# Optimization experiments

Measured on AMD Instinct MI355X. Metric: run time of the kernel, lower is better.

The kernel has to match this reference:

```python
import jax, jax.numpy as jnp
import numpy as np

HEAD_DIM = 128
MROPE_SECTION = (16, 24, 24)  # sums to HEAD_DIM // 2
ROPE_THETA = 1000000.0
NEG_INF = -2.3819763e38


def _mrope_cos_sin(positions, theta, mrope_section, head_dim):
    # positions: [3, B, T] int; returns cos, sin of shape [B, T, head_dim]
    half = head_dim // 2
    inv_freq = 1.0 / (theta ** (jnp.arange(half, dtype=jnp.float32) * 2.0 / head_dim))
    angles = positions.astype(jnp.float32)[..., None] * inv_freq  # [3, B, T, half]
    sec = np.cumsum([0] + list(mrope_section))
    # pick temporal/height/width channel per frequency band
    angles_sel = jnp.concatenate(
        [angles[j, ..., sec[j]:sec[j + 1]] for j in range(3)], axis=-1
    )  # [B, T, half]
    cos = jnp.cos(angles_sel)
    sin = jnp.sin(angles_sel)
    cos = jnp.concatenate([cos, cos], axis=-1)  # [B, T, head_dim]
    sin = jnp.concatenate([sin, sin], axis=-1)
    return cos, sin


def _apply_rope(x, cos, sin):
    # x: [B, T, n, H]; cos/sin: [B, T, H]
    half = x.shape[-1] // 2
    x1, x2 = x[..., :half], x[..., half:]
    rot = jnp.concatenate([-x2, x1], axis=-1)
    return x * cos[:, :, None, :] + rot * sin[:, :, None, :]


def setup_inputs() -> dict:
    key = jax.random.key(0)
    ks = jax.random.split(key, 8)
    B, T, D = 2, 512, 3584
    N, K, H = 28, 4, 128
    S_CACHE = 3584
    S = S_CACHE + T
    x = jax.random.normal(ks[0], (B, T, D), dtype=jnp.float32)
    wq = jax.random.normal(ks[1], (N, D, H), dtype=jnp.float32) * (D ** -0.5)
    wk = jax.random.normal(ks[2], (K, D, H), dtype=jnp.float32) * (D ** -0.5)
    wv = jax.random.normal(ks[3], (K, D, H), dtype=jnp.float32) * (D ** -0.5)
    wo = jax.random.normal(ks[4], (N, H, D), dtype=jnp.float32) * ((N * H) ** -0.5)
    cache_k = jax.random.normal(ks[5], (B, S_CACHE, K, H), dtype=jnp.float32)
    cache_v = jax.random.normal(ks[6], (B, S_CACHE, K, H), dtype=jnp.float32)
    # positions continue after the cache; all 3 mrope channels identical (text)
    pos1d = S_CACHE + jnp.arange(T, dtype=jnp.int32)
    positions = jnp.broadcast_to(pos1d[None, None, :], (3, B, T))
    # mask: full visibility into cache, causal within the new block
    causal = jnp.tril(jnp.ones((T, T), dtype=bool))
    attn_mask = jnp.concatenate(
        [jnp.ones((T, S_CACHE), dtype=bool), causal], axis=-1
    )[None, None].repeat(B, axis=0)  # [B, 1, T, S]
    return {"x": x, "positions": positions, "attn_mask": attn_mask,
            "cache_k": cache_k, "cache_v": cache_v,
            "wq": wq, "wk": wk, "wv": wv, "wo": wo}


def reference(x, positions, attn_mask, cache_k, cache_v, wq, wk, wv, wo):
    N, K, H = wq.shape[0], wk.shape[0], wq.shape[2]
    G = N // K
    q = jnp.einsum('BTD,NDH->BTNH', x, wq)
    k = jnp.einsum('BSD,KDH->BSKH', x, wk)
    v = jnp.einsum('BSD,KDH->BSKH', x, wv)
    cos, sin = _mrope_cos_sin(positions, ROPE_THETA, MROPE_SECTION, H)
    q = _apply_rope(q, cos, sin)
    k = _apply_rope(k, cos, sin)
    q = q * (H ** -0.5)
    k = jnp.concatenate([cache_k, k], axis=1)  # [B, S, K, H]
    v = jnp.concatenate([cache_v, v], axis=1)
    cached_k, cached_v = k, v
    B, T = q.shape[0], q.shape[1]
    qg = q.reshape(B, T, K, G, H)
    # GQA: broadcast each kv head over its G query-head group (same math as repeat_kv)
    logits = jnp.einsum('BTKGH,BSKH->BKGTS', qg, k,
                        preferred_element_type=jnp.float32)
    masked = jnp.where(attn_mask[:, :, None, :, :], logits, NEG_INF)
    probs = jax.nn.softmax(masked, axis=-1).astype(x.dtype)
    encoded = jnp.einsum('BKGTS,BSKH->BTKGH', probs, v).reshape(B, T, N, H)
    out = jnp.einsum('BTNH,NHD->BTD', encoded, wo)
    return out, cached_k, cached_v
```

## Files before the change

kernel.cpp:

```cpp
#include <hip/hip_runtime.h>
#include <cstdint>
#include <cstddef>
#include <cmath>

typedef __bf16 bf16;
typedef __bf16 bf16x8 __attribute__((ext_vector_type(8)));
typedef float f32x4 __attribute__((ext_vector_type(4)));

__device__ __forceinline__ f32x4 mfma_bf16(bf16x8 a, bf16x8 b, f32x4 c) {
  return __builtin_amdgcn_mfma_f32_16x16x32_bf16(a, b, c, 0, 0, 0);
}

union U8 { bf16 h[8]; uint4 u; };
__device__ __forceinline__ uint4 cvt8(float4 a, float4 b) {
  U8 t;
  t.h[0] = (bf16)a.x; t.h[1] = (bf16)a.y; t.h[2] = (bf16)a.z; t.h[3] = (bf16)a.w;
  t.h[4] = (bf16)b.x; t.h[5] = (bf16)b.y; t.h[6] = (bf16)b.z; t.h[7] = (bf16)b.w;
  return t.u;
}

__device__ __forceinline__ bf16x8 ones8() {
  union { uint4 u; bf16x8 h; } t;
  t.u = make_uint4(0x3F803F80u, 0x3F803F80u, 0x3F803F80u, 0x3F803F80u);
  return t.h;
}

__device__ __forceinline__ void gload_lds16(const bf16* g, bf16* l) {
  __builtin_amdgcn_global_load_lds((const __attribute__((address_space(1))) void*)g,
                                   (__attribute__((address_space(3))) void*)l, 16, 0, 0);
}

__global__ __launch_bounds__(256) void prep(const float* __restrict__ ck,
                                            const float* __restrict__ cv,
                                            float* __restrict__ cko,
                                            float* __restrict__ cvo,
                                            bf16* __restrict__ kb_t,
                                            const float* __restrict__ x,
                                            bf16* __restrict__ xb,
                                            const int* __restrict__ pos,
                                            float* __restrict__ cosb,
                                            float* __restrict__ sinb) {
  size_t idx = (size_t)blockIdx.x * 256 + threadIdx.x;
  size_t e = idx * 8;
  size_t b = e / 1835008u, re = e % 1835008u;
  size_t de = b * 2097152u + re;
  float4 k0 = *(const float4*)(ck + e), k1 = *(const float4*)(ck + e + 4);
  float4 v0 = *(const float4*)(cv + e), v1 = *(const float4*)(cv + e + 4);
  *(float4*)(cko + de) = k0; *(float4*)(cko + de + 4) = k1;
  *(float4*)(cvo + de) = v0; *(float4*)(cvo + de + 4) = v1;
  {
    int s = (int)(re >> 9);
    int rem = (int)(re & 511);
    int khh = rem >> 7, h0 = rem & 127;
    size_t dk = ((size_t)(b * 4 + khh) * 128 + (s >> 5)) * 4096 + (size_t)(s & 31) * 128 + h0;
    *(uint4*)(kb_t + dk) = cvt8(k0, k1);
  }
  *(uint4*)(xb + e) = cvt8(*(const float4*)(x + e), *(const float4*)(x + e + 4));
  if (idx < 65536) {
    int m = (int)(idx >> 6), i = (int)(idx & 63);
    int j = (i < 16) ? 0 : ((i < 40) ? 1 : 2);
    float p = (float)pos[j * 1024 + m];
    float invf = (float)exp((double)i * -0.21586735246819178);
    float a = p * invf;
    cosb[m * 64 + i] = cosf(a);
    sinb[m * 64 + i] = sinf(a);
  }
}

__global__ __launch_bounds__(256) void transpose_f2b(const float* __restrict__ src,
                                                     bf16* __restrict__ dst,
                                                     int R, int C) {
  const size_t ms = (size_t)R * C;
  const float* s = src + (size_t)blockIdx.z * ms;
  bf16* d = dst + (size_t)blockIdx.z * ms;
  const int c0 = blockIdx.x * 64, r0 = blockIdx.y * 64;
  __shared__ bf16 tile[64 * 72];
  const int tid = threadIdx.x;
#pragma unroll
  for (int it = 0; it < 2; ++it) {
    int slot = tid + it * 256;
    int r = slot >> 3, c8 = slot & 7;
    const float* p = s + (size_t)(r0 + r) * C + c0 + c8 * 8;
    *(uint4*)(tile + r * 72 + c8 * 8) = cvt8(*(const float4*)p, *(const float4*)(p + 4));
  }
  __syncthreads();
#pragma unroll
  for (int it = 0; it < 2; ++it) {
    int slot = tid + it * 256;
    int c = slot >> 3, r8 = slot & 7;
    U8 tmp;
#pragma unroll
    for (int jj = 0; jj < 8; ++jj) tmp.h[jj] = tile[(r8 * 8 + jj) * 72 + c];
    *(uint4*)(d + (size_t)(c0 + c) * R + r0 + r8 * 8) = tmp.u;
  }
}

__global__ __launch_bounds__(256) void transpose_qkv(const float* __restrict__ wq,
                                                     const float* __restrict__ wk,
                                                     const float* __restrict__ wv,
                                                     bf16* __restrict__ dst) {
  const size_t ms = (size_t)3584 * 128;
  const int z = blockIdx.z;
  const float* s = (z < 28) ? wq + (size_t)z * ms
                 : (z < 32) ? wk + (size_t)(z - 28) * ms
                            : wv + (size_t)(z - 32) * ms;
  bf16* d = dst + (size_t)z * ms;
  const int c0 = blockIdx.x * 64, r0 = blockIdx.y * 64;
  __shared__ bf16 tile[64 * 72];
  const int tid = threadIdx.x;
#pragma unroll
  for (int it = 0; it < 2; ++it) {
    int slot = tid + it * 256;
    int r = slot >> 3, c8 = slot & 7;
    const float* p = s + (size_t)(r0 + r) * 128 + c0 + c8 * 8;
    *(uint4*)(tile + r * 72 + c8 * 8) = cvt8(*(const float4*)p, *(const float4*)(p + 4));
  }
  __syncthreads();
#pragma unroll
  for (int it = 0; it < 2; ++it) {
    int slot = tid + it * 256;
    int c = slot >> 3, r8 = slot & 7;
    U8 tmp;
#pragma unroll
    for (int jj = 0; jj < 8; ++jj) tmp.h[jj] = tile[(r8 * 8 + jj) * 72 + c];
    *(uint4*)(d + (size_t)(c0 + c) * 3584 + r0 + r8 * 8) = tmp.u;
  }
}

__global__ __launch_bounds__(256) void transpose_v(const float* __restrict__ cvo,
                                                   bf16* __restrict__ vt_t) {
  const int b = blockIdx.z >> 2, kh = blockIdx.z & 3;
  const int s0 = blockIdx.x * 64, h0 = blockIdx.y * 64;
  __shared__ bf16 tile[64 * 72];
  const int tid = threadIdx.x;
#pragma unroll
  for (int it = 0; it < 2; ++it) {
    int slot = tid + it * 256;
    int r = slot >> 3, c8 = slot & 7;
    const float* p = cvo + (size_t)((b * 4096 + s0 + r) * 4 + kh) * 128 + h0 + c8 * 8;
    *(uint4*)(tile + r * 72 + c8 * 8) = cvt8(*(const float4*)p, *(const float4*)(p + 4));
  }
  __syncthreads();
#pragma unroll
  for (int it = 0; it < 2; ++it) {
    int slot = tid + it * 256;
    int c = slot >> 3, r8 = slot & 7;
    U8 tmp;
#pragma unroll
    for (int jj = 0; jj < 8; ++jj) tmp.h[jj] = tile[(r8 * 8 + jj) * 72 + c];
    int s = s0 + r8 * 8;
    *(uint4*)(vt_t + ((size_t)((b * 4 + kh) * 128 + (s >> 5))) * 4096 +
              (size_t)(h0 + c) * 32 + (s & 31)) = tmp.u;
  }
}

template <int MODE>
__global__ __launch_bounds__(256) void gemm128(
    const bf16* __restrict__ A, const bf16* __restrict__ Bt,
    bf16* __restrict__ q_ws, float* __restrict__ cko, bf16* __restrict__ kb_t,
    float* __restrict__ cvo, const float* __restrict__ cosb,
    const float* __restrict__ sinb, float* __restrict__ outp) {
  const int cb = blockIdx.x;
  const int m0 = blockIdx.y * 128;
  const int tid = threadIdx.x;
  const int wave = tid >> 6, lane = tid & 63;
  const int c16 = lane & 15, q4 = lane >> 4;
  __shared__ bf16 lA[2][128 * 64];
  __shared__ bf16 lB[2][128 * 64];

  int offA[2][2], offB[8][2];
#pragma unroll
  for (int i = 0; i < 2; ++i) {
    int rA = wave * 32 + i * 16 + c16;
#pragma unroll
    for (int kk = 0; kk < 2; ++kk) offA[i][kk] = rA * 64 + (kk * 4 + q4) * 8;
  }
#pragma unroll
  for (int j = 0; j < 8; ++j) {
    int rB = j * 16 + c16;
#pragma unroll
    for (int kk = 0; kk < 2; ++kk) offB[j][kk] = rB * 64 + (kk * 4 + q4) * 8;
  }

  f32x4 acc[2][8];
#pragma unroll
  for (int i = 0; i < 2; ++i)
#pragma unroll
    for (int j = 0; j < 8; ++j) acc[i][j] = (f32x4){0.f, 0.f, 0.f, 0.f};

#pragma unroll
  for (int it = 0; it < 4; ++it) {
    int slot = tid + it * 256;
    gload_lds16(A + (size_t)(m0 + (slot >> 3)) * 3584 + (slot & 7) * 8, &lA[0][slot * 8]);
    gload_lds16(Bt + (size_t)(cb * 128 + (slot >> 3)) * 3584 + (slot & 7) * 8, &lB[0][slot * 8]);
  }
  __syncthreads();

  for (int k0 = 0; k0 < 3584; k0 += 64) {
    const int cur = (k0 >> 6) & 1;
    if (k0 + 64 < 3584) {
#pragma unroll
      for (int it = 0; it < 4; ++it) {
        int slot = tid + it * 256;
        gload_lds16(A + (size_t)(m0 + (slot >> 3)) * 3584 + k0 + 64 + (slot & 7) * 8,
                    &lA[cur ^ 1][slot * 8]);
        gload_lds16(Bt + (size_t)(cb * 128 + (slot >> 3)) * 3584 + k0 + 64 + (slot & 7) * 8,
                    &lB[cur ^ 1][slot * 8]);
      }
    }
#pragma unroll
    for (int kk = 0; kk < 2; ++kk) {
      bf16x8 av0 = *(const bf16x8*)(&lA[cur][offA[0][kk]]);
      bf16x8 av1 = *(const bf16x8*)(&lA[cur][offA[1][kk]]);
#pragma unroll
      for (int j = 0; j < 8; ++j) {
        bf16x8 bv = *(const bf16x8*)(&lB[cur][offB[j][kk]]);
        acc[0][j] = mfma_bf16(av0, bv, acc[0][j]);
        acc[1][j] = mfma_bf16(av1, bv, acc[1][j]);
      }
    }
    __syncthreads();
  }

  if (MODE == 1) {
#pragma unroll
    for (int i = 0; i < 2; ++i) {
      int mb = m0 + wave * 32 + i * 16 + q4 * 4;
#pragma unroll
      for (int r = 0; r < 4; ++r) {
        size_t rowoff = (size_t)(mb + r) * 3584 + cb * 128;
#pragma unroll
        for (int j = 0; j < 8; ++j) outp[rowoff + j * 16 + c16] = acc[i][j][r];
      }
    }
    return;
  }

  const int head = cb;
#pragma unroll
  for (int i = 0; i < 2; ++i) {
    int mb = m0 + wave * 32 + i * 16 + q4 * 4;
#pragma unroll
    for (int r = 0; r < 4; ++r) {
      int m = mb + r;
      int bb = m >> 9, tt = m & 511;
      if (head < 32) {
        const float* cp = cosb + m * 64;
        const float* sp = sinb + m * 64;
#pragma unroll
        for (int j = 0; j < 4; ++j) {
          int h = j * 16 + c16;
          float c = cp[h], s = sp[h];
          float v1 = acc[i][j][r], v2 = acc[i][j + 4][r];
          float o1 = v1 * c - v2 * s;
          float o2 = v2 * c + v1 * s;
          if (head < 28) {
            const float QS = 0.08838834764831845f;
            size_t base = ((size_t)m * 28 + head) * 128;
            q_ws[base + h] = (bf16)(o1 * QS);
            q_ws[base + h + 64] = (bf16)(o2 * QS);
          } else {
            int sg = 3584 + tt;
            size_t base = ((size_t)((bb * 4096 + sg) * 4 + (head - 28))) * 128;
            cko[base + h] = o1;
            cko[base + h + 64] = o2;
            size_t bt = ((size_t)(bb * 4 + (head - 28)) * 128 + (sg >> 5)) * 4096 +
                        (size_t)(sg & 31) * 128;
            kb_t[bt + h] = (bf16)o1;
            kb_t[bt + h + 64] = (bf16)o2;
          }
        }
      } else {
        size_t base = ((size_t)((bb * 4096 + 3584 + tt) * 4 + (head - 32))) * 128;
#pragma unroll
        for (int j = 0; j < 8; ++j) cvo[base + j * 16 + c16] = acc[i][j][r];
      }
    }
  }
}

__global__ __launch_bounds__(512) void attn_kernel(const bf16* __restrict__ q_ws,
                                                   const bf16* __restrict__ kb_t,
                                                   const bf16* __restrict__ vt_t,
                                                   bf16* __restrict__ enc) {
  const int combo = blockIdx.x & 7;
  const int b = combo >> 2, kh = combo & 3;
  const int t0 = (blockIdx.x >> 3) * 16;
  const int tid = threadIdx.x;
  const int wave = tid >> 6, lane = tid & 63;
  const int c16 = lane & 15, q4 = lane >> 4;

  __shared__ bf16 Kc[3][4096];
  __shared__ bf16 Vc[3][4096];
  __shared__ bf16 Ps[8][16 * 40];

  const int kr = tid >> 4, ksl = tid & 15;
  const int ksrc = kr * 128 + ((ksl ^ (kr & 7)) * 8);
  const int vh = tid >> 2, vsl = tid & 3;
  const int vsrc = vh * 32 + ((vsl ^ ((vh >> 1) & 3)) * 8);
  const bf16* kcb = kb_t + (size_t)((b * 4 + kh) * 128) * 4096;
  const bf16* vcb = vt_t + (size_t)((b * 4 + kh) * 128) * 4096;

  int koff[2][4];
#pragma unroll
  for (int kk = 0; kk < 4; ++kk) {
    int ph = ((q4 * 16 + kk * 64) ^ ((c16 & 7) << 4)) >> 1;
    koff[0][kk] = c16 * 128 + ph;
    koff[1][kk] = (c16 + 16) * 128 + ph;
  }
  int voff[8];
#pragma unroll
  for (int jo = 0; jo < 8; ++jo)
    voff[jo] = (jo * 16 + c16) * 32 + ((q4 ^ ((c16 >> 1) & 3)) * 8);

  const int n = kh * 7 + wave;
  bf16x8 aQ[4];
  if (wave < 7) {
    const bf16* qbase = q_ws + ((size_t)((b * 512 + t0 + c16) * 28 + n)) * 128 + q4 * 8;
#pragma unroll
    for (int kk = 0; kk < 4; ++kk) aQ[kk] = *(const bf16x8*)(qbase + kk * 32);
  }

  f32x4 accO[8];
  f32x4 accL = (f32x4){0.f, 0.f, 0.f, 0.f};
#pragma unroll
  for (int j = 0; j < 8; ++j) accO[j] = (f32x4){0.f, 0.f, 0.f, 0.f};
  const bf16x8 vone = ones8();
  bf16* pw = Ps[wave];

  const int nch = (3631 + t0) >> 5;

  gload_lds16(kcb + ksrc, &Kc[0][tid * 8]);
  gload_lds16(vcb + vsrc, &Vc[0][tid * 8]);
  gload_lds16(kcb + 4096 + ksrc, &Kc[1][tid * 8]);
  gload_lds16(vcb + 4096 + vsrc, &Vc[1][tid * 8]);
  asm volatile("s_waitcnt vmcnt(2)" ::: "memory");
  __builtin_amdgcn_sched_barrier(0);
  __builtin_amdgcn_s_barrier();
  __builtin_amdgcn_sched_barrier(0);

  int cur = 0, nx2 = 2;
  for (int c = 0; c < nch; ++c) {
    {
      int cn = (c + 2 < nch) ? c + 2 : nch - 1;
      gload_lds16(kcb + (size_t)cn * 4096 + ksrc, &Kc[nx2][tid * 8]);
      gload_lds16(vcb + (size_t)cn * 4096 + vsrc, &Vc[nx2][tid * 8]);
    }
    if (wave < 7) {
      const int s0 = c * 32;
      const bf16* kc = Kc[cur];
      const bf16* vc = Vc[cur];
      f32x4 accS0 = (f32x4){0.f, 0.f, 0.f, 0.f};
      f32x4 accS1 = (f32x4){0.f, 0.f, 0.f, 0.f};
#pragma unroll
      for (int kk = 0; kk < 4; ++kk) {
        bf16x8 bK0 = *(const bf16x8*)(&kc[koff[0][kk]]);
        bf16x8 bK1 = *(const bf16x8*)(&kc[koff[1][kk]]);
        accS0 = mfma_bf16(aQ[kk], bK0, accS0);
        accS1 = mfma_bf16(aQ[kk], bK1, accS1);
      }

      if (s0 + 31 > 3584 + t0) {
#pragma unroll
        for (int r = 0; r < 4; ++r) {
          int lim = 3584 + t0 + q4 * 4 + r - s0;
          float p0 = (c16 <= lim) ? __expf(accS0[r]) : 0.f;
          float p1 = (16 + c16 <= lim) ? __expf(accS1[r]) : 0.f;
          int prow = (q4 * 4 + r) * 40;
          pw[prow + c16] = (bf16)p0;
          pw[prow + 16 + c16] = (bf16)p1;
        }
      } else {
#pragma unroll
        for (int r = 0; r < 4; ++r) {
          int prow = (q4 * 4 + r) * 40;
          pw[prow + c16] = (bf16)__expf(accS0[r]);
          pw[prow + 16 + c16] = (bf16)__expf(accS1[r]);
        }
      }

      bf16x8 aP = *(const bf16x8*)(pw + c16 * 40 + q4 * 8);
      accL = mfma_bf16(aP, vone, accL);
#pragma unroll
      for (int jo = 0; jo < 8; ++jo) {
        bf16x8 bV = *(const bf16x8*)(&vc[voff[jo]]);
        accO[jo] = mfma_bf16(aP, bV, accO[jo]);
      }
    }
    asm volatile("s_waitcnt lgkmcnt(0)" ::: "memory");
    asm volatile("s_waitcnt vmcnt(2)" ::: "memory");
    __builtin_amdgcn_sched_barrier(0);
    __builtin_amdgcn_s_barrier();
    __builtin_amdgcn_sched_barrier(0);
    cur = (cur == 2) ? 0 : cur + 1;
    nx2 = (nx2 == 2) ? 0 : nx2 + 1;
  }

  if (wave < 7) {
#pragma unroll
    for (int r = 0; r < 4; ++r) {
      float inv = 1.0f / accL[r];
      int tg = t0 + q4 * 4 + r;
      size_t base = ((size_t)((b * 512 + tg) * 28 + n)) * 128;
#pragma unroll
      for (int jo = 0; jo < 8; ++jo)
        enc[base + jo * 16 + c16] = (bf16)(accO[jo][r] * inv);
    }
  }
}

extern "C" void kernel_launch(void* const* d_in, const int* in_sizes, int n_in,
                              void* d_out, int out_size, void* d_ws, size_t ws_size,
                              hipStream_t stream) {
  const float* x = (const float*)d_in[0];
  const int* pos = (const int*)d_in[1];
  const float* ck = (const float*)d_in[3];
  const float* cv = (const float*)d_in[4];
  const float* wq = (const float*)d_in[5];
  const float* wk = (const float*)d_in[6];
  const float* wv = (const float*)d_in[7];
  const float* wo = (const float*)d_in[8];

  float* out = (float*)d_out;
  float* cko = out + 3670016;
  float* cvo = cko + 4194304;

  bf16* wqkvT = (bf16*)d_ws;
  bf16* woT = wqkvT;
  bf16* xb = wqkvT + 16515072;
  bf16* q_ws = xb + 3670016;
  bf16* encw = q_ws + 3670016;
  bf16* kb_t = encw + 3670016;
  bf16* vt_t = kb_t + 4194304;
  float* cosb = (float*)(vt_t + 4194304);
  float* sinb = cosb + 65536;
  if (ws_size < 72351744ull) return;

  prep<<<1792, 256, 0, stream>>>(ck, cv, cko, cvo, kb_t, x, xb, pos, cosb, sinb);
  transpose_qkv<<<dim3(2, 56, 36), 256, 0, stream>>>(wq, wk, wv, wqkvT);
  gemm128<0><<<dim3(36, 8), 256, 0, stream>>>(xb, wqkvT, q_ws, cko, kb_t, cvo, cosb, sinb, nullptr);
  transpose_f2b<<<dim3(56, 56, 1), 256, 0, stream>>>(wo, woT, 3584, 3584);
  transpose_v<<<dim3(64, 2, 8), 256, 0, stream>>>(cvo, vt_t);
  attn_kernel<<<256, 512, 0, stream>>>(q_ws, kb_t, vt_t, encw);
  gemm128<1><<<dim3(28, 8), 256, 0, stream>>>(encw, woT, nullptr, nullptr, nullptr, nullptr,
                                              nullptr, nullptr, out);
}
```

Baseline: 502.4 us.

## Split attention KV sequence into three partitions and merge partial outputs

The attention kernel now splits each query tile's KV range into three parts and launches three times as many blocks. This raises occupancy on the many-CU GPU, since the old launch of 256 blocks underfilled it. Each part writes unnormalized bf16 partial outputs and row sums to scratch buffers that reuse workspace and the output buffer, and a new merge kernel sums them and normalizes. The pipeline also drops from triple-buffered async loads with manual waitcnt to double buffering with __syncthreads, which can expose load latency. It also adds an extra kernel launch and extra memory traffic, and summing the partials in bf16 loses some precision. Because no max is subtracted, the exp values are unbounded, which was already true before.

```diff
diff --git a/kernel.cpp b/kernel.cpp
--- a/kernel.cpp
+++ b/kernel.cpp
@@ -282,16 +282,21 @@
 __global__ __launch_bounds__(512) void attn_kernel(const bf16* __restrict__ q_ws,
                                                    const bf16* __restrict__ kb_t,
                                                    const bf16* __restrict__ vt_t,
-                                                   bf16* __restrict__ enc) {
+                                                   bf16* __restrict__ p0,
+                                                   bf16* __restrict__ p1,
+                                                   bf16* __restrict__ p2,
+                                                   float* __restrict__ lp) {
   const int combo = blockIdx.x & 7;
   const int b = combo >> 2, kh = combo & 3;
-  const int t0 = (blockIdx.x >> 3) * 16;
+  const int rest = blockIdx.x >> 3;
+  const int third = rest % 3;
+  const int t0 = (rest / 3) * 16;
   const int tid = threadIdx.x;
   const int wave = tid >> 6, lane = tid & 63;
   const int c16 = lane & 15, q4 = lane >> 4;
 
-  __shared__ bf16 Kc[3][4096];
-  __shared__ bf16 Vc[3][4096];
+  __shared__ bf16 Kc[2][4096];
+  __shared__ bf16 Vc[2][4096];
   __shared__ bf16 Ps[8][16 * 40];
 
   const int kr = tid >> 4, ksl = tid & 15;
@@ -329,22 +334,17 @@
   bf16* pw = Ps[wave];
 
   const int nch = (3631 + t0) >> 5;
-
-  gload_lds16(kcb + ksrc, &Kc[0][tid * 8]);
-  gload_lds16(vcb + vsrc, &Vc[0][tid * 8]);
-  gload_lds16(kcb + 4096 + ksrc, &Kc[1][tid * 8]);
-  gload_lds16(vcb + 4096 + vsrc, &Vc[1][tid * 8]);
-  asm volatile("s_waitcnt vmcnt(2)" ::: "memory");
-  __builtin_amdgcn_sched_barrier(0);
-  __builtin_amdgcn_s_barrier();
-  __builtin_amdgcn_sched_barrier(0);
-
-  int cur = 0, nx2 = 2;
-  for (int c = 0; c < nch; ++c) {
-    {
-      int cn = (c + 2 < nch) ? c + 2 : nch - 1;
-      gload_lds16(kcb + (size_t)cn * 4096 + ksrc, &Kc[nx2][tid * 8]);
-      gload_lds16(vcb + (size_t)cn * 4096 + vsrc, &Vc[nx2][tid * 8]);
+  const int lo = (nch * third) / 3, hi = (nch * (third + 1)) / 3;
+
+  gload_lds16(kcb + (size_t)lo * 4096 + ksrc, &Kc[0][tid * 8]);
+  gload_lds16(vcb + (size_t)lo * 4096 + vsrc, &Vc[0][tid * 8]);
+  __syncthreads();
+
+  for (int c = lo; c < hi; ++c) {
+    const int cur = (c - lo) & 1;
+    if (c + 1 < hi) {
+      gload_lds16(kcb + (size_t)(c + 1) * 4096 + ksrc, &Kc[cur ^ 1][tid * 8]);
+      gload_lds16(vcb + (size_t)(c + 1) * 4096 + vsrc, &Vc[cur ^ 1][tid * 8]);
     }
     if (wave < 7) {
       const int s0 = c * 32;
@@ -364,11 +364,11 @@
 #pragma unroll
         for (int r = 0; r < 4; ++r) {
           int lim = 3584 + t0 + q4 * 4 + r - s0;
-          float p0 = (c16 <= lim) ? __expf(accS0[r]) : 0.f;
-          float p1 = (16 + c16 <= lim) ? __expf(accS1[r]) : 0.f;
+          float x0 = (c16 <= lim) ? __expf(accS0[r]) : 0.f;
+          float x1 = (16 + c16 <= lim) ? __expf(accS1[r]) : 0.f;
           int prow = (q4 * 4 + r) * 40;
-          pw[prow + c16] = (bf16)p0;
-          pw[prow + 16 + c16] = (bf16)p1;
+          pw[prow + c16] = (bf16)x0;
+          pw[prow + 16 + c16] = (bf16)x1;
         }
       } else {
 #pragma unroll
@@ -387,26 +387,42 @@
         accO[jo] = mfma_bf16(aP, bV, accO[jo]);
       }
     }
-    asm volatile("s_waitcnt lgkmcnt(0)" ::: "memory");
-    asm volatile("s_waitcnt vmcnt(2)" ::: "memory");
-    __builtin_amdgcn_sched_barrier(0);
-    __builtin_amdgcn_s_barrier();
-    __builtin_amdgcn_sched_barrier(0);
-    cur = (cur == 2) ? 0 : cur + 1;
-    nx2 = (nx2 == 2) ? 0 : nx2 + 1;
+    __syncthreads();
   }
 
   if (wave < 7) {
+    bf16* pb = (third == 0) ? p0 : (third == 1) ? p1 : p2;
 #pragma unroll
     for (int r = 0; r < 4; ++r) {
-      float inv = 1.0f / accL[r];
       int tg = t0 + q4 * 4 + r;
-      size_t base = ((size_t)((b * 512 + tg) * 28 + n)) * 128;
+      size_t row = (size_t)(b * 512 + tg) * 28 + n;
+      size_t base = row * 128;
 #pragma unroll
       for (int jo = 0; jo < 8; ++jo)
-        enc[base + jo * 16 + c16] = (bf16)(accO[jo][r] * inv);
-    }
-  }
+        pb[base + jo * 16 + c16] = (bf16)accO[jo][r];
+      if (c16 == 0) lp[third * 57344 + row] = accL[r];
+    }
+  }
+}
+
+__global__ __launch_bounds__(256) void attn_merge(const bf16* __restrict__ p0,
+                                                  const bf16* __restrict__ p1,
+                                                  const bf16* __restrict__ p2,
+                                                  const float* __restrict__ lp,
+                                                  bf16* __restrict__ enc) {
+  size_t idx = (size_t)blockIdx.x * 256 + threadIdx.x;
+  size_t e = idx * 8;
+  size_t row = e >> 7;
+  float l = lp[row] + lp[57344 + row] + lp[114688 + row];
+  float inv = 1.0f / l;
+  bf16x8 a = *(const bf16x8*)(p0 + e);
+  bf16x8 b8 = *(const bf16x8*)(p1 + e);
+  bf16x8 c8 = *(const bf16x8*)(p2 + e);
+  U8 o;
+#pragma unroll
+  for (int j = 0; j < 8; ++j)
+    o.h[j] = (bf16)(((float)a[j] + (float)b8[j] + (float)c8[j]) * inv);
+  *(uint4*)(enc + e) = o.u;
 }
 
 extern "C" void kernel_launch(void* const* d_in, const int* in_sizes, int n_in,
@@ -427,6 +443,7 @@
 
   bf16* wqkvT = (bf16*)d_ws;
   bf16* woT = wqkvT;
+  bf16* p2 = wqkvT + 12845056;
   bf16* xb = wqkvT + 16515072;
   bf16* q_ws = xb + 3670016;
   bf16* encw = q_ws + 3670016;
@@ -434,6 +451,7 @@
   bf16* vt_t = kb_t + 4194304;
   float* cosb = (float*)(vt_t + 4194304);
   float* sinb = cosb + 65536;
+  float* lp = out;
   if (ws_size < 72351744ull) return;
 
   prep<<<1792, 256, 0, stream>>>(ck, cv, cko, cvo, kb_t, x, xb, pos, cosb, sinb);
@@ -441,7 +459,8 @@
   gemm128<0><<<dim3(36, 8), 256, 0, stream>>>(xb, wqkvT, q_ws, cko, kb_t, cvo, cosb, sinb, nullptr);
   transpose_f2b<<<dim3(56, 56, 1), 256, 0, stream>>>(wo, woT, 3584, 3584);
   transpose_v<<<dim3(64, 2, 8), 256, 0, stream>>>(cvo, vt_t);
-  attn_kernel<<<256, 512, 0, stream>>>(q_ws, kb_t, vt_t, encw);
+  attn_kernel<<<768, 512, 0, stream>>>(q_ws, kb_t, vt_t, encw, xb, p2, lp);
+  attn_merge<<<1792, 256, 0, stream>>>(encw, xb, p2, lp, encw);
   gemm128<1><<<dim3(28, 8), 256, 0, stream>>>(encw, woT, nullptr, nullptr, nullptr, nullptr,
                                               nullptr, nullptr, out);
 }
```

After: 471.9 us. 6.1% less time.
